# Kernel tuning notes

Hardware: AMD Instinct MI355X
Metric: run time of the kernel (lower is better)

## Reference

```python
import jax, jax.numpy as jnp
import numpy as np

B, CIN, COUT, N, R = 8, 64, 64, 32768, 32
R3 = R * R * R
BN_EPS = 1e-4


def leaky(x):
    return jnp.where(x >= 0, x, 0.1 * x)


def bn(x, gamma, beta, axes, bshape):
    # training-mode batchnorm (batch statistics)
    m = x.mean(axes, keepdims=True)
    v = x.var(axes, keepdims=True)
    return (x - m) * jax.lax.rsqrt(v + BN_EPS) * gamma.reshape(bshape) + beta.reshape(bshape)


def conv3d(x, w, b):
    y = jax.lax.conv_general_dilated(
        x, w, window_strides=(1, 1, 1), padding=[(1, 1)] * 3,
        dimension_numbers=('NCDHW', 'OIDHW', 'NCDHW'))
    return y + b[None, :, None, None, None]


def setup_inputs() -> dict:
    key = jax.random.key(0)
    ks = jax.random.split(key, 6)
    f32 = jnp.float32
    return {
        'features': jax.random.normal(ks[0], (B, CIN, N), f32),
        'coords': jax.random.normal(ks[1], (B, 3, N), f32),
        'w1': jax.random.normal(ks[2], (COUT, CIN, 3, 3, 3), f32) * 0.05,
        'b1': jnp.zeros((COUT,), f32),
        'g1': jnp.ones((COUT,), f32),
        'beta1': jnp.zeros((COUT,), f32),
        'w2': jax.random.normal(ks[3], (COUT, COUT, 3, 3, 3), f32) * 0.05,
        'b2': jnp.zeros((COUT,), f32),
        'g2': jnp.ones((COUT,), f32),
        'beta2': jnp.zeros((COUT,), f32),
        'wp': jax.random.normal(ks[4], (COUT, CIN), f32) * 0.05,
        'bp': jnp.zeros((COUT,), f32),
        'gp': jnp.ones((COUT,), f32),
        'betap': jnp.zeros((COUT,), f32),
    }


def _norm_coords(coords):
    # Voxelization coordinate normalization (normalize=True, eps=0)
    nc = coords - coords.mean(axis=2, keepdims=True)                      # [B,3,N]
    mag = jnp.linalg.norm(nc, axis=1, keepdims=True)                      # [B,1,N]
    nc = nc / (mag.max(axis=2, keepdims=True) * 2.0) + 0.5
    return jnp.clip(nc * R, 0.0, R - 1)                                   # [B,3,N] in [0, R-1]


def _voxelize(features, norm):
    vox = jnp.round(norm).astype(jnp.int32)                               # [B,3,N]
    flat = (vox[:, 0] * R + vox[:, 1]) * R + vox[:, 2]                    # [B,N]

    def scat(f, idx):  # f: [C,N], idx: [N]
        s = jax.ops.segment_sum(f.T, idx, num_segments=R3)                # [R3,C]
        c = jax.ops.segment_sum(jnp.ones(idx.shape, f.dtype), idx, num_segments=R3)
        return (s / jnp.maximum(c, 1.0)[:, None]).T                       # [C,R3]

    return jax.vmap(scat)(features, flat)                                 # [B,C,R3]


def _devoxelize(grid_flat, norm):
    # trilinear gather: grid_flat [B,C,R3], norm [B,3,N] -> [B,C,N]
    lo = jnp.floor(norm).astype(jnp.int32)
    frac = norm - lo
    hi = jnp.clip(lo + 1, 0, R - 1)
    gather = jax.vmap(lambda gf, i: gf[:, i])  # per-batch fancy gather
    out = jnp.zeros((grid_flat.shape[0], grid_flat.shape[1], norm.shape[2]), grid_flat.dtype)
    for dx in (0, 1):
        for dy in (0, 1):
            for dz in (0, 1):
                xi = hi[:, 0] if dx else lo[:, 0]
                yi = hi[:, 1] if dy else lo[:, 1]
                zi = hi[:, 2] if dz else lo[:, 2]
                w = ((frac[:, 0] if dx else 1.0 - frac[:, 0]) *
                     (frac[:, 1] if dy else 1.0 - frac[:, 1]) *
                     (frac[:, 2] if dz else 1.0 - frac[:, 2]))            # [B,N]
                idx = (xi * R + yi) * R + zi                               # [B,N]
                out = out + gather(grid_flat, idx) * w[:, None, :]
    return out


def reference(features, coords, w1, b1, g1, beta1, w2, b2, g2, beta2, wp, bp, gp, betap):
    norm = _norm_coords(coords)
    grid = _voxelize(features, norm).reshape(B, CIN, R, R, R)
    x = leaky(bn(conv3d(grid, w1, b1), g1, beta1, (0, 2, 3, 4), (1, COUT, 1, 1, 1)))
    x = leaky(bn(conv3d(x, w2, b2), g2, beta2, (0, 2, 3, 4), (1, COUT, 1, 1, 1)))
    voxel_feats = _devoxelize(x.reshape(B, COUT, R3), norm)               # [B,COUT,N]
    # point branch: SharedMLP = 1x1 Conv1d + BN1d + ReLU
    p = jnp.einsum('oc,bcn->bon', wp, features) + bp[None, :, None]
    p = jax.nn.relu(bn(p, gp, betap, (0, 2), (1, COUT, 1)))
    return voxel_feats + p
```

## Files before the change

kernel.cpp:

```cpp
#include <hip/hip_runtime.h>

typedef __attribute__((ext_vector_type(8))) short short8;
typedef __attribute__((ext_vector_type(8))) unsigned short ushort8;
typedef __attribute__((ext_vector_type(4))) unsigned short ushort4v;
typedef __attribute__((ext_vector_type(4))) float f32x4;
typedef unsigned int uint;
typedef unsigned short ushort;

#define BB 8
#define CC 64
#define NPT 32768
#define RR 32
#define R3 32768
#define RP 34
#define RP2 1156
#define RP3 39304
#define BN_EPS 1e-4f

__device__ __forceinline__ ushort f2bf(float x) {
    uint u = __float_as_uint(x);
    u = (u + 0x7FFFu + ((u >> 16) & 1u)) >> 16;
    return (ushort)u;
}
__device__ __forceinline__ float bf2f(ushort u) {
    return __uint_as_float(((uint)u) << 16);
}
__device__ __forceinline__ void gload_lds16(const void* g, void* l) {
    __builtin_amdgcn_global_load_lds(
        (const __attribute__((address_space(1))) unsigned int*)g,
        (__attribute__((address_space(3))) unsigned int*)l, 16, 0, 0);
}

__global__ void k_mean(const float* __restrict__ coords, float* __restrict__ mean) {
    __shared__ float sbuf[256];
    int bd = blockIdx.x;
    const float* c = coords + (size_t)bd * NPT;
    float s = 0.f;
    for (int i = threadIdx.x; i < NPT; i += 256) s += c[i];
    sbuf[threadIdx.x] = s; __syncthreads();
    for (int off = 128; off > 0; off >>= 1) {
        if (threadIdx.x < off) sbuf[threadIdx.x] += sbuf[threadIdx.x + off];
        __syncthreads();
    }
    if (threadIdx.x == 0) mean[bd] = sbuf[0] / (float)NPT;
}

__global__ void k_maxmag(const float* __restrict__ coords, const float* __restrict__ mean,
                         float* __restrict__ maxmag) {
    __shared__ float sbuf[256];
    int b = blockIdx.x;
    float m0 = mean[b*3], m1 = mean[b*3+1], m2 = mean[b*3+2];
    const float* c = coords + (size_t)b * 3 * NPT;
    float mx = 0.f;
    for (int i = threadIdx.x; i < NPT; i += 256) {
        float x = c[i] - m0, y = c[NPT + i] - m1, z = c[2*NPT + i] - m2;
        mx = fmaxf(mx, x*x + y*y + z*z);
    }
    sbuf[threadIdx.x] = mx; __syncthreads();
    for (int off = 128; off > 0; off >>= 1) {
        if (threadIdx.x < off) sbuf[threadIdx.x] = fmaxf(sbuf[threadIdx.x], sbuf[threadIdx.x + off]);
        __syncthreads();
    }
    if (threadIdx.x == 0) maxmag[b] = sqrtf(sbuf[0]);
}

__global__ void k_norm(const float* __restrict__ coords, const float* __restrict__ mean,
                       const float* __restrict__ maxmag,
                       float* __restrict__ norm, int* __restrict__ nxt, int* __restrict__ head) {
    int b = blockIdx.y;
    int n = blockIdx.x * 256 + threadIdx.x;
    float denom = maxmag[b] * 2.0f;
    int vi[3];
    #pragma unroll
    for (int d = 0; d < 3; d++) {
        float v = (coords[((size_t)b*3 + d)*NPT + n] - mean[b*3 + d]) / denom + 0.5f;
        v *= (float)RR;
        v = fminf(fmaxf(v, 0.0f), (float)(RR - 1));
        norm[((size_t)b*3 + d)*NPT + n] = v;
        vi[d] = (int)rintf(v);
    }
    int pf = ((vi[0]+1)*RP + (vi[1]+1))*RP + (vi[2]+1);
    nxt[b*NPT + n] = atomicExch(&head[b*RP3 + pf], n);
}

__global__ __launch_bounds__(256) void k_transpose(const float* __restrict__ feat,
                                                   float* __restrict__ featT) {
    __shared__ float t[64][65];
    int b = blockIdx.y;
    int n0 = blockIdx.x * 64;
    for (int i = threadIdx.x; i < 4096; i += 256) {
        int ci = i >> 6, nl = i & 63;
        t[ci][nl] = feat[((size_t)(b*CC + ci))*NPT + n0 + nl];
    }
    __syncthreads();
    for (int i = threadIdx.x; i < 4096; i += 256) {
        int nl = i >> 6, ci = i & 63;
        featT[((size_t)b*NPT + n0 + nl)*64 + ci] = t[ci][nl];
    }
}

__global__ __launch_bounds__(256) void k_gather(const float* __restrict__ featT,
                                                const int* __restrict__ head,
                                                const int* __restrict__ nxt,
                                                ushort* __restrict__ gbf) {
    int b = blockIdx.y;
    int v = blockIdx.x * 4 + (threadIdx.x >> 6);
    int lane = threadIdx.x & 63;
    float a = 0.f;
    int c = 0;
    int p = head[b*RP3 + v];
    while (p >= 0) {
        a += featT[((size_t)b*NPT + p)*64 + lane];
        c++;
        p = nxt[b*NPT + p];
    }
    float r = (c > 0) ? a / (float)c : 0.f;
    gbf[((size_t)((b*2 + (lane >> 5))*RP3) + v)*32 + (lane & 31)] = f2bf(r);
}

__global__ void k_wt(const float* __restrict__ w, ushort* __restrict__ wT) {
    int s = blockIdx.x * 256 + threadIdx.x;
    int ci = s & 31;
    int co = (s >> 5) & 63;
    int t  = (s >> 11) % 27;
    int ch = s / 55296;
    wT[s] = f2bf(w[(size_t)co*1728 + (size_t)(ch*32 + ci)*27 + t]);
}

__global__ void k_bnpack(const ushort* __restrict__ raw, const float* __restrict__ sc,
                         const float* __restrict__ sh, ushort* __restrict__ gbf) {
    int s = blockIdx.x * 256 + threadIdx.x;
    int j = s & 3;
    int tmp = s >> 2;
    int v = tmp % RP3;
    int t2 = tmp / RP3;
    int ch = t2 & 1, b = t2 >> 1;
    int gz = v / RP2; int r = v - gz*RP2;
    int gy = r / RP;  int gx = r - gy*RP;
    ushort8 o;
    if (gz >= 1 && gz <= 32 && gy >= 1 && gy <= 32 && gx >= 1 && gx <= 32) {
        int uvox = ((gz-1)*RR + (gy-1))*RR + (gx-1);
        int cb = ch*32 + j*8;
        ushort8 rv = *(const ushort8*)(raw + ((size_t)b*R3 + uvox)*64 + cb);
        f32x4 s0 = *(const f32x4*)(sc + cb), s1 = *(const f32x4*)(sc + cb + 4);
        f32x4 h0 = *(const f32x4*)(sh + cb), h1 = *(const f32x4*)(sh + cb + 4);
        #pragma unroll
        for (int e = 0; e < 4; e++) {
            float x0 = bf2f(rv[e])*s0[e] + h0[e];     x0 = x0 >= 0.f ? x0 : 0.1f*x0;
            float x1 = bf2f(rv[4+e])*s1[e] + h1[e];   x1 = x1 >= 0.f ? x1 : 0.1f*x1;
            o[e] = f2bf(x0); o[4+e] = f2bf(x1);
        }
    } else {
        #pragma unroll
        for (int e = 0; e < 8; e++) o[e] = 0;
    }
    *(ushort8*)(gbf + ((size_t)((b*2 + ch)*RP3) + v)*32 + j*8) = o;
}

__global__ __launch_bounds__(512) void k_conv_mfma(
    const ushort* __restrict__ gbf,
    const ushort* __restrict__ wT,
    ushort* __restrict__ rawbf,
    float* __restrict__ gs, float* __restrict__ gq)
{
    __shared__ uint4 lds4[2 * 3888];
    const int d0r = blockIdx.x;
    const int d0 = (d0r & 7) * 4 + (d0r >> 3);
    const int quad = blockIdx.y, b = blockIdx.z;
    const int y0 = (quad >> 1) * 16, x0 = (quad & 1) * 16;
    const int tid = threadIdx.x;
    const int lane = tid & 63;
    const int wid = tid >> 6;
    const int mgroup = wid & 1, ngroup = wid >> 1;
    const int l15 = lane & 15, kgrp = lane >> 4;

    f32x4 acc[2][4];
    #pragma unroll
    for (int mf = 0; mf < 2; mf++)
        #pragma unroll
        for (int f = 0; f < 4; f++) acc[mf][f] = (f32x4)(0.0f);

    const int coA = mgroup*32 + l15;
    const int coB = coA + 16;

    {
        const char* gbase = (const char*)gbf + (size_t)(b*2 + 0) * ((size_t)RP3 * 64);
        for (int c = tid; c < 3888; c += 512) {
            int row = c >> 2, j = c & 3;
            int z = row / 324; int rem = row - z*324;
            int y = rem / 18;  int xl = rem - y*18;
            int srcj = j ^ ((xl >> 1) & 3);
            const char* src = gbase +
                (size_t)((d0 + z)*RP2 + (y0 + y)*RP + (x0 + xl)) * 64 + srcj*16;
            gload_lds16(src, (char*)lds4 + c*16);
        }
    }
    __syncthreads();
    {
        const char* gbase = (const char*)gbf + (size_t)(b*2 + 1) * ((size_t)RP3 * 64);
        for (int c = tid; c < 3888; c += 512) {
            int row = c >> 2, j = c & 3;
            int z = row / 324; int rem = row - z*324;
            int y = rem / 18;  int xl = rem - y*18;
            int srcj = j ^ ((xl >> 1) & 3);
            const char* src = gbase +
                (size_t)((d0 + z)*RP2 + (y0 + y)*RP + (x0 + xl)) * 64 + srcj*16;
            gload_lds16(src, (char*)lds4 + 62208 + c*16);
        }
    }

    #pragma unroll
    for (int ch = 0; ch < 2; ch++) {
        if (ch == 1) __syncthreads();
        const char* lbase = (const char*)lds4 + ch * 62208;
        const ushort* wbase = wT + (size_t)ch * 27 * 2048 + kgrp*8;
        short8 wq[3][2];
        #pragma unroll
        for (int pre = 0; pre < 3; pre++) {
            wq[pre][0] = *(const short8*)(wbase + (size_t)pre*2048 + coA*32);
            wq[pre][1] = *(const short8*)(wbase + (size_t)pre*2048 + coB*32);
        }
        __builtin_amdgcn_s_setprio(1);
        #pragma unroll
        for (int t = 0; t < 27; t++) {
            const int t0 = t / 9, t1 = (t / 3) % 3, t2 = t % 3;
            const int slot = t % 3;
            int x = l15 + t2;
            int inrow = (kgrp ^ ((x >> 1) & 3)) << 4;
            #pragma unroll
            for (int f = 0; f < 4; f++) {
                int y = ngroup*4 + f + t1;
                int vox = (t0*18 + y)*18 + x;
                short8 bfr = *(const short8*)(lbase + vox*64 + inrow);
                acc[0][f] = __builtin_amdgcn_mfma_f32_16x16x32_bf16(wq[slot][0], bfr, acc[0][f], 0, 0, 0);
                acc[1][f] = __builtin_amdgcn_mfma_f32_16x16x32_bf16(wq[slot][1], bfr, acc[1][f], 0, 0, 0);
            }
            if (t + 3 < 27) {
                wq[slot][0] = *(const short8*)(wbase + (size_t)(t+3)*2048 + coA*32);
                wq[slot][1] = *(const short8*)(wbase + (size_t)(t+3)*2048 + coB*32);
            }
        }
        __builtin_amdgcn_s_setprio(0);
    }
    int d2 = x0 + l15;
    #pragma unroll
    for (int f = 0; f < 4; f++) {
        int d1 = y0 + ngroup*4 + f;
        int vox = (d0*RR + d1)*RR + d2;
        ushort* dst = rawbf + ((size_t)b*R3 + vox)*64 + mgroup*32 + kgrp*4;
        ushort4v o0, o1;
        #pragma unroll
        for (int e = 0; e < 4; e++) { o0[e] = f2bf(acc[0][f][e]); o1[e] = f2bf(acc[1][f][e]); }
        *(ushort4v*)dst = o0;
        *(ushort4v*)(dst + 16) = o1;
    }
    __syncthreads();
    float* bins = (float*)lds4;
    if (tid < 128) bins[tid] = 0.f;
    __syncthreads();
    float sv[2][4], qv[2][4];
    #pragma unroll
    for (int mf = 0; mf < 2; mf++)
        #pragma unroll
        for (int e = 0; e < 4; e++) {
            float s = 0.f, q = 0.f;
            #pragma unroll
            for (int f = 0; f < 4; f++) {
                float v = acc[mf][f][e];
                s += v; q += v*v;
            }
            #pragma unroll
            for (int m = 1; m < 16; m <<= 1) {
                s += __shfl_xor(s, m);
                q += __shfl_xor(q, m);
            }
            sv[mf][e] = s; qv[mf][e] = q;
        }
    if (l15 == 0) {
        #pragma unroll
        for (int mf = 0; mf < 2; mf++)
            #pragma unroll
            for (int e = 0; e < 4; e++) {
                int co = mgroup*32 + mf*16 + kgrp*4 + e;
                atomicAdd(&bins[co], sv[mf][e]);
                atomicAdd(&bins[64 + co], qv[mf][e]);
            }
    }
    __syncthreads();
    if (tid < 64) { atomicAdd(&gs[tid], bins[tid]); atomicAdd(&gq[tid], bins[64 + tid]); }
}

__global__ void k_finalize(const float* __restrict__ ssum, const float* __restrict__ ssq,
                           const float* __restrict__ gamma, const float* __restrict__ beta,
                           float* __restrict__ scale, float* __restrict__ shift) {
    int c = threadIdx.x;
    const float cntf = 262144.0f;
    float m = ssum[c] / cntf;
    float v = ssq[c] / cntf - m*m;
    float sc = gamma[c] * rsqrtf(fmaxf(v, 0.0f) + BN_EPS);
    scale[c] = sc;
    shift[c] = beta[c] - m*sc;
}

__global__ __launch_bounds__(256) void k_point_stats_P(const float* __restrict__ featT,
                                                       const float* __restrict__ wp,
                                                       ushort* __restrict__ P,
                                                       float* __restrict__ gs,
                                                       float* __restrict__ gq) {
    __shared__ float ls[64], lq[64];
    int b = blockIdx.y;
    int n = blockIdx.x * 256 + threadIdx.x;
    if (threadIdx.x < 64) { ls[threadIdx.x] = 0.f; lq[threadIdx.x] = 0.f; }
    __syncthreads();
    f32x4 fr[16];
    const f32x4* fp = (const f32x4*)(featT + ((size_t)b*NPT + n)*64);
    #pragma unroll
    for (int r = 0; r < 16; r++) fr[r] = fp[r];
    int lane = threadIdx.x & 63;
    #pragma unroll
    for (int co = 0; co < 64; co++) {
        float p = 0.f;
        #pragma unroll
        for (int r = 0; r < 16; r++) {
            f32x4 w4 = *(const f32x4*)(wp + co*64 + r*4);
            p = fmaf(w4[0], fr[r][0], p); p = fmaf(w4[1], fr[r][1], p);
            p = fmaf(w4[2], fr[r][2], p); p = fmaf(w4[3], fr[r][3], p);
        }
        P[((size_t)(b*64 + co))*NPT + n] = f2bf(p);
        float s = p, q = p*p;
        #pragma unroll
        for (int m = 1; m < 64; m <<= 1) {
            s += __shfl_xor(s, m);
            q += __shfl_xor(q, m);
        }
        if (lane == 0) { atomicAdd(&ls[co], s); atomicAdd(&lq[co], q); }
    }
    __syncthreads();
    if (threadIdx.x < 64) {
        atomicAdd(&gs[threadIdx.x], ls[threadIdx.x]);
        atomicAdd(&gq[threadIdx.x], lq[threadIdx.x]);
    }
}

__global__ __launch_bounds__(256) void k_final4(
    const ushort* __restrict__ x2raw,
    const float* __restrict__ norm,
    const ushort* __restrict__ P,
    const float* __restrict__ sc2, const float* __restrict__ sh2,
    const float* __restrict__ scp, const float* __restrict__ shp,
    float* __restrict__ out)
{
    __shared__ float s_sc[64], s_sh[64];
    int b = blockIdx.y;
    int tid = threadIdx.x;
    if (tid < 64) { s_sc[tid] = sc2[tid]; s_sh[tid] = sh2[tid]; }
    __syncthreads();
    int pt = blockIdx.x * 64 + (tid & 63);
    int q = tid >> 6;
    float v0 = norm[((size_t)b*3 + 0)*NPT + pt];
    float v1 = norm[((size_t)b*3 + 1)*NPT + pt];
    float v2 = norm[((size_t)b*3 + 2)*NPT + pt];
    int l0 = (int)floorf(v0), l1 = (int)floorf(v1), l2 = (int)floorf(v2);
    float f0 = v0 - (float)l0, f1 = v1 - (float)l1, f2 = v2 - (float)l2;
    int h0 = min(l0 + 1, RR - 1), h1 = min(l1 + 1, RR - 1), h2 = min(l2 + 1, RR - 1);

    f32x4 scv[4], shv[4];
    #pragma unroll
    for (int r = 0; r < 4; r++) {
        scv[r] = *(const f32x4*)&s_sc[q*16 + r*4];
        shv[r] = *(const f32x4*)&s_sh[q*16 + r*4];
    }

    f32x4 a4[4];
    #pragma unroll
    for (int r = 0; r < 4; r++) a4[r] = (f32x4)(0.0f);
    #pragma unroll
    for (int c = 0; c < 8; c++) {
        int xi = (c & 4) ? h0 : l0; float wx = (c & 4) ? f0 : 1.f - f0;
        int yi = (c & 2) ? h1 : l1; float wy = (c & 2) ? f1 : 1.f - f1;
        int zi = (c & 1) ? h2 : l2; float wz = (c & 1) ? f2 : 1.f - f2;
        float w = wx * wy * wz;
        const ushort* g = x2raw +
            ((size_t)b*R3 + (size_t)((xi*RR + yi)*RR + zi))*64 + q*16;
        ushort8 rv0 = *(const ushort8*)g;
        ushort8 rv1 = *(const ushort8*)(g + 8);
        #pragma unroll
        for (int r = 0; r < 2; r++) {
            #pragma unroll
            for (int e = 0; e < 4; e++) {
                float x = bf2f(rv0[r*4 + e])*scv[r][e] + shv[r][e];
                x = x >= 0.f ? x : 0.1f*x;
                a4[r][e] = fmaf(w, x, a4[r][e]);
                float x2 = bf2f(rv1[r*4 + e])*scv[2 + r][e] + shv[2 + r][e];
                x2 = x2 >= 0.f ? x2 : 0.1f*x2;
                a4[2 + r][e] = fmaf(w, x2, a4[2 + r][e]);
            }
        }
    }
    #pragma unroll
    for (int r = 0; r < 4; r++) {
        #pragma unroll
        for (int e = 0; e < 4; e++) {
            int co = q*16 + r*4 + e;
            float p = bf2f(P[((size_t)(b*64 + co))*NPT + pt]);
            p = p * scp[co] + shp[co];
            p = fmaxf(p, 0.f);
            out[((size_t)(b*64 + co))*NPT + pt] = a4[r][e] + p;
        }
    }
}

extern "C" void kernel_launch(void* const* d_in, const int* in_sizes, int n_in,
                              void* d_out, int out_size, void* d_ws, size_t ws_size,
                              hipStream_t stream) {
    const float* feat   = (const float*)d_in[0];
    const float* coords = (const float*)d_in[1];
    const float* w1  = (const float*)d_in[2];
    const float* g1  = (const float*)d_in[4];
    const float* be1 = (const float*)d_in[5];
    const float* w2  = (const float*)d_in[6];
    const float* g2  = (const float*)d_in[8];
    const float* be2 = (const float*)d_in[9];
    const float* wp  = (const float*)d_in[10];
    const float* gp  = (const float*)d_in[12];
    const float* bep = (const float*)d_in[13];
    float* out = (float*)d_out;
    float* ws  = (float*)d_ws;

    float* mean   = ws;
    float* maxmag = ws + 24;
    float* stats  = ws + 32;
    float* sc     = ws + 416;
    float* norm   = ws + 1024;
    int*   nxt    = (int*)(ws + 787456);
    int*   head   = (int*)(ws + 1049600);
    ushort* rawbf = (ushort*)(ws + 1364032);
    ushort* wT1   = (ushort*)(ws + 21487680);
    ushort* wT2   = (ushort*)(ws + 21542976);
    ushort* gbf   = (ushort*)(ws + 21598272);
    ushort* P     = (ushort*)(ws + 21598272);
    float* featT  = ws + 31660096;

    hipMemsetAsync(stats, 0, 384 * sizeof(float), stream);
    hipMemsetAsync(head, 0xFF, 314432ull * sizeof(int), stream);

    k_wt<<<432, 256, 0, stream>>>(w1, wT1);
    k_wt<<<432, 256, 0, stream>>>(w2, wT2);

    k_mean  <<<24, 256, 0, stream>>>(coords, mean);
    k_maxmag<<<8, 256, 0, stream>>>(coords, mean, maxmag);
    k_norm  <<<dim3(128, 8), 256, 0, stream>>>(coords, mean, maxmag, norm, nxt, head);
    k_transpose<<<dim3(512, 8), 256, 0, stream>>>(feat, featT);
    k_gather<<<dim3(9826, 8), 256, 0, stream>>>(featT, head, nxt, gbf);

    k_conv_mfma<<<dim3(32, 4, 8), 512, 0, stream>>>(gbf, wT1, rawbf, stats + 0, stats + 64);
    k_finalize<<<1, 64, 0, stream>>>(stats + 0, stats + 64, g1, be1, sc + 0, sc + 64);
    k_bnpack<<<9826, 256, 0, stream>>>(rawbf, sc + 0, sc + 64, gbf);

    k_conv_mfma<<<dim3(32, 4, 8), 512, 0, stream>>>(gbf, wT2, rawbf, stats + 128, stats + 192);
    k_finalize<<<1, 64, 0, stream>>>(stats + 128, stats + 192, g2, be2, sc + 128, sc + 192);

    k_point_stats_P<<<dim3(128, 8), 256, 0, stream>>>(featT, wp, P, stats + 256, stats + 320);
    k_finalize<<<1, 64, 0, stream>>>(stats + 256, stats + 320, gp, bep, sc + 256, sc + 320);

    k_final4<<<dim3(512, 8), 256, 0, stream>>>(rawbf, norm, P, sc + 128, sc + 192,
                                               sc + 256, sc + 320, out);
}
```

Before: 529.6 us.

## Store transposed features in bf16 and fuse BN finalize into consumer kernels

The transposed point-feature buffer is now written and read as bf16 instead of fp32. This halves the memory traffic of the transpose, the voxel gather and the point MLP stats kernel. The separate BN finalize kernels are removed, and each consumer (bnpack, final) computes scale and shift from the accumulated sums into shared memory, saving three tiny launches. The cost is lower precision of the input features before averaging and the 1x1 conv, plus redundant per-block finalize arithmetic.

Result: faster. 494.8 us (-6.6%).

```diff
diff --git a/kernel.cpp b/kernel.cpp
--- a/kernel.cpp
+++ b/kernel.cpp
@@ -84,7 +84,7 @@
 }
 
 __global__ __launch_bounds__(256) void k_transpose(const float* __restrict__ feat,
-                                                   float* __restrict__ featT) {
+                                                   ushort* __restrict__ featT) {
     __shared__ float t[64][65];
     int b = blockIdx.y;
     int n0 = blockIdx.x * 64;
@@ -95,11 +95,11 @@
     __syncthreads();
     for (int i = threadIdx.x; i < 4096; i += 256) {
         int nl = i >> 6, ci = i & 63;
-        featT[((size_t)b*NPT + n0 + nl)*64 + ci] = t[ci][nl];
-    }
-}
-
-__global__ __launch_bounds__(256) void k_gather(const float* __restrict__ featT,
+        featT[((size_t)b*NPT + n0 + nl)*64 + ci] = f2bf(t[ci][nl]);
+    }
+}
+
+__global__ __launch_bounds__(256) void k_gather(const ushort* __restrict__ featT,
                                                 const int* __restrict__ head,
                                                 const int* __restrict__ nxt,
                                                 ushort* __restrict__ gbf) {
@@ -110,7 +110,7 @@
     int c = 0;
     int p = head[b*RP3 + v];
     while (p >= 0) {
-        a += featT[((size_t)b*NPT + p)*64 + lane];
+        a += bf2f(featT[((size_t)b*NPT + p)*64 + lane]);
         c++;
         p = nxt[b*NPT + p];
     }
@@ -127,8 +127,21 @@
     wT[s] = f2bf(w[(size_t)co*1728 + (size_t)(ch*32 + ci)*27 + t]);
 }
 
-__global__ void k_bnpack(const ushort* __restrict__ raw, const float* __restrict__ sc,
-                         const float* __restrict__ sh, ushort* __restrict__ gbf) {
+__global__ void k_bnpack(const ushort* __restrict__ raw,
+                         const float* __restrict__ gs, const float* __restrict__ gq,
+                         const float* __restrict__ gamma, const float* __restrict__ beta,
+                         ushort* __restrict__ gbf) {
+    __shared__ float s_sc[64], s_sh[64];
+    if (threadIdx.x < 64) {
+        int c = threadIdx.x;
+        const float cntf = 262144.0f;
+        float m = gs[c] / cntf;
+        float vv = gq[c] / cntf - m*m;
+        float scv = gamma[c] * rsqrtf(fmaxf(vv, 0.0f) + BN_EPS);
+        s_sc[c] = scv;
+        s_sh[c] = beta[c] - m*scv;
+    }
+    __syncthreads();
     int s = blockIdx.x * 256 + threadIdx.x;
     int j = s & 3;
     int tmp = s >> 2;
@@ -142,13 +155,11 @@
         int uvox = ((gz-1)*RR + (gy-1))*RR + (gx-1);
         int cb = ch*32 + j*8;
         ushort8 rv = *(const ushort8*)(raw + ((size_t)b*R3 + uvox)*64 + cb);
-        f32x4 s0 = *(const f32x4*)(sc + cb), s1 = *(const f32x4*)(sc + cb + 4);
-        f32x4 h0 = *(const f32x4*)(sh + cb), h1 = *(const f32x4*)(sh + cb + 4);
-        #pragma unroll
-        for (int e = 0; e < 4; e++) {
-            float x0 = bf2f(rv[e])*s0[e] + h0[e];     x0 = x0 >= 0.f ? x0 : 0.1f*x0;
-            float x1 = bf2f(rv[4+e])*s1[e] + h1[e];   x1 = x1 >= 0.f ? x1 : 0.1f*x1;
-            o[e] = f2bf(x0); o[4+e] = f2bf(x1);
+        #pragma unroll
+        for (int e = 0; e < 8; e++) {
+            float x = bf2f(rv[e])*s_sc[cb + e] + s_sh[cb + e];
+            x = x >= 0.f ? x : 0.1f*x;
+            o[e] = f2bf(x);
         }
     } else {
         #pragma unroll
@@ -290,19 +301,7 @@
     if (tid < 64) { atomicAdd(&gs[tid], bins[tid]); atomicAdd(&gq[tid], bins[64 + tid]); }
 }
 
-__global__ void k_finalize(const float* __restrict__ ssum, const float* __restrict__ ssq,
-                           const float* __restrict__ gamma, const float* __restrict__ beta,
-                           float* __restrict__ scale, float* __restrict__ shift) {
-    int c = threadIdx.x;
-    const float cntf = 262144.0f;
-    float m = ssum[c] / cntf;
-    float v = ssq[c] / cntf - m*m;
-    float sc = gamma[c] * rsqrtf(fmaxf(v, 0.0f) + BN_EPS);
-    scale[c] = sc;
-    shift[c] = beta[c] - m*sc;
-}
-
-__global__ __launch_bounds__(256) void k_point_stats_P(const float* __restrict__ featT,
+__global__ __launch_bounds__(256) void k_point_stats_P(const ushort* __restrict__ featT,
                                                        const float* __restrict__ wp,
                                                        ushort* __restrict__ P,
                                                        float* __restrict__ gs,
@@ -313,9 +312,14 @@
     if (threadIdx.x < 64) { ls[threadIdx.x] = 0.f; lq[threadIdx.x] = 0.f; }
     __syncthreads();
     f32x4 fr[16];
-    const f32x4* fp = (const f32x4*)(featT + ((size_t)b*NPT + n)*64);
-    #pragma unroll
-    for (int r = 0; r < 16; r++) fr[r] = fp[r];
+    const ushort8* fp = (const ushort8*)(featT + ((size_t)b*NPT + n)*64);
+    #pragma unroll
+    for (int r = 0; r < 8; r++) {
+        ushort8 u = fp[r];
+        #pragma unroll
+        for (int e = 0; e < 8; e++)
+            fr[(r*8 + e) >> 2][(r*8 + e) & 3] = bf2f(u[e]);
+    }
     int lane = threadIdx.x & 63;
     #pragma unroll
     for (int co = 0; co < 64; co++) {
@@ -346,14 +350,29 @@
     const ushort* __restrict__ x2raw,
     const float* __restrict__ norm,
     const ushort* __restrict__ P,
-    const float* __restrict__ sc2, const float* __restrict__ sh2,
-    const float* __restrict__ scp, const float* __restrict__ shp,
+    const float* __restrict__ gs2, const float* __restrict__ gq2,
+    const float* __restrict__ g2, const float* __restrict__ be2,
+    const float* __restrict__ gsp, const float* __restrict__ gqp,
+    const float* __restrict__ gp, const float* __restrict__ bep,
     float* __restrict__ out)
 {
-    __shared__ float s_sc[64], s_sh[64];
+    __shared__ float s_sc[64], s_sh[64], s_scp[64], s_shp[64];
     int b = blockIdx.y;
     int tid = threadIdx.x;
-    if (tid < 64) { s_sc[tid] = sc2[tid]; s_sh[tid] = sh2[tid]; }
+    const float cntf = 262144.0f;
+    if (tid < 64) {
+        int c = tid;
+        float m = gs2[c] / cntf;
+        float vv = gq2[c] / cntf - m*m;
+        float scv = g2[c] * rsqrtf(fmaxf(vv, 0.0f) + BN_EPS);
+        s_sc[c] = scv; s_sh[c] = be2[c] - m*scv;
+    } else if (tid < 128) {
+        int c = tid - 64;
+        float m = gsp[c] / cntf;
+        float vv = gqp[c] / cntf - m*m;
+        float scv = gp[c] * rsqrtf(fmaxf(vv, 0.0f) + BN_EPS);
+        s_scp[c] = scv; s_shp[c] = bep[c] - m*scv;
+    }
     __syncthreads();
     int pt = blockIdx.x * 64 + (tid & 63);
     int q = tid >> 6;
@@ -403,7 +422,7 @@
         for (int e = 0; e < 4; e++) {
             int co = q*16 + r*4 + e;
             float p = bf2f(P[((size_t)(b*64 + co))*NPT + pt]);
-            p = p * scp[co] + shp[co];
+            p = p * s_scp[co] + s_shp[co];
             p = fmaxf(p, 0.f);
             out[((size_t)(b*64 + co))*NPT + pt] = a4[r][e] + p;
         }
@@ -430,7 +449,6 @@
     float* mean   = ws;
     float* maxmag = ws + 24;
     float* stats  = ws + 32;
-    float* sc     = ws + 416;
     float* norm   = ws + 1024;
     int*   nxt    = (int*)(ws + 787456);
     int*   head   = (int*)(ws + 1049600);
@@ -439,7 +457,7 @@
     ushort* wT2   = (ushort*)(ws + 21542976);
     ushort* gbf   = (ushort*)(ws + 21598272);
     ushort* P     = (ushort*)(ws + 21598272);
-    float* featT  = ws + 31660096;
+    ushort* featT = (ushort*)(ws + 31660096);
 
     hipMemsetAsync(stats, 0, 384 * sizeof(float), stream);
     hipMemsetAsync(head, 0xFF, 314432ull * sizeof(int), stream);
@@ -454,15 +472,14 @@
     k_gather<<<dim3(9826, 8), 256, 0, stream>>>(featT, head, nxt, gbf);
 
     k_conv_mfma<<<dim3(32, 4, 8), 512, 0, stream>>>(gbf, wT1, rawbf, stats + 0, stats + 64);
-    k_finalize<<<1, 64, 0, stream>>>(stats + 0, stats + 64, g1, be1, sc + 0, sc + 64);
-    k_bnpack<<<9826, 256, 0, stream>>>(rawbf, sc + 0, sc + 64, gbf);
+    k_bnpack<<<9826, 256, 0, stream>>>(rawbf, stats + 0, stats + 64, g1, be1, gbf);
 
     k_conv_mfma<<<dim3(32, 4, 8), 512, 0, stream>>>(gbf, wT2, rawbf, stats + 128, stats + 192);
-    k_finalize<<<1, 64, 0, stream>>>(stats + 128, stats + 192, g2, be2, sc + 128, sc + 192);
 
     k_point_stats_P<<<dim3(128, 8), 256, 0, stream>>>(featT, wp, P, stats + 256, stats + 320);
-    k_finalize<<<1, 64, 0, stream>>>(stats + 256, stats + 320, gp, bep, sc + 256, sc + 320);
-
-    k_final4<<<dim3(512, 8), 256, 0, stream>>>(rawbf, norm, P, sc + 128, sc + 192,
-                                               sc + 256, sc + 320, out);
-}
+
+    k_final4<<<dim3(512, 8), 256, 0, stream>>>(rawbf, norm, P,
+                                               stats + 128, stats + 192, g2, be2,
+                                               stats + 256, stats + 320, gp, bep,
+                                               out);
+}
```
